# Kernel tuning notes

Hardware: AMD Instinct MI355X
Metric: run time of the kernel (lower is better)

## Reference

```python
import jax, jax.numpy as jnp
from jax import lax
import numpy as np

B, Q, T, C = 64, 900, 100, 92
W_CLASS, W_BBOX, W_GIOU = 1.0, 1.0, 1.0


def to_corners(b):
    cx, cy, w, h = b[..., 0], b[..., 1], b[..., 2], b[..., 3]
    return jnp.stack([cx - 0.5 * w, cy - 0.5 * h, cx + 0.5 * w, cy + 0.5 * h], axis=-1)


def generalized_iou(b1, b2):
    # b1 [Q,4], b2 [T,4] in corner format -> pairwise GIoU [Q,T]
    a1 = (b1[:, 2] - b1[:, 0]) * (b1[:, 3] - b1[:, 1])
    a2 = (b2[:, 2] - b2[:, 0]) * (b2[:, 3] - b2[:, 1])
    lt = jnp.maximum(b1[:, None, :2], b2[None, :, :2])
    rb = jnp.minimum(b1[:, None, 2:], b2[None, :, 2:])
    wh = jnp.clip(rb - lt, 0.0)
    inter = wh[..., 0] * wh[..., 1]
    union = a1[:, None] + a2[None, :] - inter
    iou = inter / union
    lt_e = jnp.minimum(b1[:, None, :2], b2[None, :, :2])
    rb_e = jnp.maximum(b1[:, None, 2:], b2[None, :, 2:])
    wh_e = jnp.clip(rb_e - lt_e, 0.0)
    area_e = wh_e[..., 0] * wh_e[..., 1]
    return iou - (area_e - union) / area_e


def cost_matrix(logits, pred_bbox, tgt_labels, tgt_bbox):
    conf = jax.nn.softmax(logits, axis=-1)                                  # [B,Q,C]
    cost_class = -jax.vmap(lambda c, l: c[:, l])(conf, tgt_labels)          # [B,Q,T]
    cost_bbox = jnp.sum(jnp.abs(pred_bbox[:, :, None, :] - tgt_bbox[:, None, :, :]), axis=-1)
    cost_giou = -jax.vmap(generalized_iou)(to_corners(pred_bbox), to_corners(tgt_bbox))
    return W_BBOX * cost_bbox + W_CLASS * cost_class + W_GIOU * cost_giou   # [B,Q,T]


def solve_lsa(cost):
    # Jonker-Volgenant shortest-augmenting-path optimal assignment.
    # cost [n, m] with n <= m; assigns every row to a distinct column.
    n, m = cost.shape
    INF = jnp.asarray(1e9, cost.dtype)

    def assign_row(i, carry):
        u, v, p = carry        # u [n+1], v [m+1] potentials; p [m+1]: row assigned to col (0=free)
        p = p.at[0].set(i + 1)
        minv0 = jnp.full(m + 1, INF, cost.dtype)
        used0 = jnp.zeros(m + 1, bool)
        way0 = jnp.zeros(m + 1, jnp.int32)

        def cond(s):
            j0, u, v, p, minv, used, way = s
            return p[j0] != 0

        def body(s):
            j0, u, v, p, minv, used, way = s
            used = used.at[j0].set(True)
            i0 = p[j0]
            cur = cost[i0 - 1] - u[i0] - v[1:]          # reduced costs over cols 1..m
            cur = jnp.where(used[1:], INF, cur)
            better = cur < minv[1:]
            minv = minv.at[1:].set(jnp.where(better, cur, minv[1:]))
            way = way.at[1:].set(jnp.where(better, j0, way[1:]))
            masked = jnp.where(used[1:], INF, minv[1:])
            j1 = jnp.argmin(masked).astype(jnp.int32) + 1
            delta = masked[j1 - 1]
            u = u.at[p].add(jnp.where(used, delta, jnp.zeros((), cost.dtype)))
            v = v - jnp.where(used, delta, jnp.zeros((), cost.dtype))
            minv = minv - jnp.where(used, jnp.zeros((), cost.dtype), delta)
            return j1, u, v, p, minv, used, way

        j0, u, v, p, _, _, way = lax.while_loop(
            cond, body, (jnp.int32(0), u, v, p, minv0, used0, way0))

        def aug_cond(s):
            jj, p = s
            return jj != 0

        def aug_body(s):
            jj, p = s
            j1 = way[jj]
            p = p.at[jj].set(p[j1])
            return j1, p

        _, p = lax.while_loop(aug_cond, aug_body, (j0, p))
        return u, v, p

    u0 = jnp.zeros(n + 1, cost.dtype)
    v0 = jnp.zeros(m + 1, cost.dtype)
    p0 = jnp.zeros(m + 1, jnp.int32)
    _, _, p = lax.fori_loop(0, n, assign_row, (u0, v0, p0))
    # column (0-based) assigned to each row i
    q = jnp.argmax(p[1:, None] == (jnp.arange(n, dtype=jnp.int32) + 1)[None, :], axis=0)
    order = jnp.argsort(q)
    return q[order].astype(jnp.int32), order.astype(jnp.int32)


def setup_inputs() -> dict:
    key = jax.random.key(0)
    k1, k2, k3, k4 = jax.random.split(key, 4)
    return {
        'logits': jax.random.normal(k1, (B, Q, C), jnp.float32),
        'pred_bbox': jax.random.uniform(k2, (B, Q, 4), jnp.float32),
        'tgt_labels': jax.random.randint(k3, (B, T), 0, C, jnp.int32),
        'tgt_bbox': jax.random.uniform(k4, (B, T, 4), jnp.float32),
    }


def reference(logits, pred_bbox, tgt_labels, tgt_bbox):
    cost = cost_matrix(logits, pred_bbox, tgt_labels, tgt_bbox)   # [B,Q,T]
    # scipy solves the [Q,T] problem (Q > T): transpose so rows (targets) <= cols (queries).
    row_ind, col_ind = jax.vmap(lambda c: solve_lsa(c.T))(cost)
    # row_ind: query indices (ascending), col_ind: matched target indices, per image.
    return cost, row_ind, col_ind
```

## Files before the change

kernel.cpp:

```cpp
#include <hip/hip_runtime.h>
#include <cmath>

#define Bq 64
#define Qn 900
#define Tn 100
#define Cn 92
#define INFN 1e9f
#define QT 64
#define NQT 15

__device__ inline unsigned fkey(float x) {
    unsigned u = __float_as_uint(x);
    return (u & 0x80000000u) ? ~u : (u | 0x80000000u);
}
__device__ inline float unfkey(unsigned k) {
    unsigned u = (k & 0x80000000u) ? (k & 0x7FFFFFFFu) : ~k;
    return __uint_as_float(u);
}

__device__ inline unsigned wave_min_u32(unsigned x) {
    unsigned t;
#define DPPSTEP(ctrl)                                                          \
    t = (unsigned)__builtin_amdgcn_update_dpp((int)0xFFFFFFFF, (int)x, ctrl,   \
                                              0xF, 0xF, false);                \
    x = (t < x) ? t : x;
    DPPSTEP(0x111)
    DPPSTEP(0x112)
    DPPSTEP(0x114)
    DPPSTEP(0x118)
    DPPSTEP(0x142)
    DPPSTEP(0x143)
#undef DPPSTEP
    return (unsigned)__builtin_amdgcn_readlane((int)x, 63);
}

__global__ __launch_bounds__(256) void cost_fused_kernel(
        const float* __restrict__ logits,
        const float* __restrict__ pred_bbox,
        const int*   __restrict__ tgt_labels,
        const float* __restrict__ tgt_bbox,
        float* __restrict__ cost,
        float* __restrict__ costT,
        unsigned long long* __restrict__ tilemin)
{
    const int b   = blockIdx.y;
    const int q0  = blockIdx.x * QT;
    const int nq  = (q0 + QT <= Qn) ? QT : (Qn - q0);
    const int tid = threadIdx.x;

    __shared__ float prob[QT * Cn];
    __shared__ float pb_s[QT][4];
    __shared__ float tb_s[Tn][4];
    __shared__ int   lab_s[Tn];
    __shared__ float ctile[QT][Tn + 1];

    const float* lg_src = logits + ((size_t)b * Qn + q0) * Cn;
    for (int idx = tid; idx < nq * Cn; idx += 256) prob[idx] = lg_src[idx];
    for (int idx = tid; idx < nq * 4; idx += 256)
        ((float*)pb_s)[idx] = pred_bbox[((size_t)b * Qn + q0) * 4 + idx];
    for (int idx = tid; idx < Tn * 4; idx += 256)
        ((float*)tb_s)[idx] = tgt_bbox[(size_t)b * Tn * 4 + idx];
    for (int idx = tid; idx < Tn; idx += 256)
        lab_s[idx] = tgt_labels[b * Tn + idx];
    __syncthreads();

    const int g = tid >> 2, l4 = tid & 3;
    if (g < nq) {
        float mx = -3.0e38f;
        for (int c = l4; c < Cn; c += 4) mx = fmaxf(mx, prob[g * Cn + c]);
        mx = fmaxf(mx, __shfl_xor(mx, 1));
        mx = fmaxf(mx, __shfl_xor(mx, 2));
        float s = 0.0f;
        for (int c = l4; c < Cn; c += 4) {
            float e = expf(prob[g * Cn + c] - mx);
            prob[g * Cn + c] = e;
            s += e;
        }
        s += __shfl_xor(s, 1);
        s += __shfl_xor(s, 2);
        float inv = 1.0f / s;
        for (int c = l4; c < Cn; c += 4) prob[g * Cn + c] *= inv;
    }
    __syncthreads();

    const int total = nq * Tn;
    float* cdst = cost + (size_t)b * Qn * Tn + (size_t)q0 * Tn;
    for (int flat = tid; flat < total; flat += 256) {
        int q = flat / Tn, tt = flat - q * Tn;
        float pcx = pb_s[q][0], pcy = pb_s[q][1], pw = pb_s[q][2], ph = pb_s[q][3];
        float tcx = tb_s[tt][0], tcy = tb_s[tt][1], tw = tb_s[tt][2], th = tb_s[tt][3];

        float cclass = -prob[q * Cn + lab_s[tt]];
        float cbbox  = fabsf(pcx - tcx) + fabsf(pcy - tcy)
                     + fabsf(pw - tw)  + fabsf(ph - th);

        float px1 = pcx - 0.5f * pw, py1 = pcy - 0.5f * ph;
        float px2 = pcx + 0.5f * pw, py2 = pcy + 0.5f * ph;
        float tx1 = tcx - 0.5f * tw, ty1 = tcy - 0.5f * th;
        float tx2 = tcx + 0.5f * tw, ty2 = tcy + 0.5f * th;

        float a1 = (px2 - px1) * (py2 - py1);
        float a2 = (tx2 - tx1) * (ty2 - ty1);
        float iw = fmaxf(fminf(px2, tx2) - fmaxf(px1, tx1), 0.0f);
        float ih = fmaxf(fminf(py2, ty2) - fmaxf(py1, ty1), 0.0f);
        float inter = iw * ih;
        float uni = a1 + a2 - inter;
        float iou = inter / uni;
        float ew = fmaxf(fmaxf(px2, tx2) - fminf(px1, tx1), 0.0f);
        float eh = fmaxf(fmaxf(py2, ty2) - fminf(py1, ty1), 0.0f);
        float ae = ew * eh;
        float val = cbbox + cclass - (iou - (ae - uni) / ae);

        cdst[flat] = val;
        ctile[q][tt] = val;
    }
    __syncthreads();

    if (costT) {
        float* tdst = costT + (size_t)b * Qn * Tn + q0;
        if (nq == QT) {
            for (int flat = tid; flat < QT * Tn; flat += 256) {
                int r = flat >> 6, c = flat & 63;
                tdst[(size_t)r * Qn + c] = ctile[c][r];
            }
        } else {
            for (int flat = tid; flat < nq * Tn; flat += 256) {
                int r = flat / nq, c = flat - r * nq;
                tdst[(size_t)r * Qn + c] = ctile[c][r];
            }
        }
    }
    if (tilemin && tid < Tn) {
        float bvv = 3.0e38f; int bq = 0;
        for (int q = 0; q < nq; ++q) {
            float x = ctile[q][tid];
            if (x < bvv) { bvv = x; bq = q; }
        }
        tilemin[((size_t)b * NQT + blockIdx.x) * Tn + tid] =
            ((unsigned long long)fkey(bvv) << 32) | (unsigned)(q0 + bq);
    }
}

template<bool TM>
__global__ __launch_bounds__(256) void jv_kernel(
        const float* __restrict__ costT,
        const unsigned long long* __restrict__ tilemin,
        float* __restrict__ out)
{
    const int b    = blockIdx.x;
    const int tid  = threadIdx.x;
    const int lane = tid & 63;
    const int wv   = tid >> 6;

    __shared__ int   p_lds[Qn + 1];
    __shared__ int   way_lds[1024];
    __shared__ float u_lds[Tn + 1];
    __shared__ int   amin_lds[Tn];
    __shared__ unsigned char asg[Tn];
    __shared__ int   freelist[Tn];
    __shared__ int   nfree_s;
    __shared__ int   qarr[Tn];

    for (int j = tid; j <= Qn; j += 256) p_lds[j] = 0;
    if (tid == 0) nfree_s = 0;
    __syncthreads();

    const float* cb = costT + (size_t)b * Qn * Tn;

    if (TM) {
        if (tid < Tn) {
            unsigned long long best = ~0ull;
            for (int t = 0; t < NQT; ++t) {
                unsigned long long v = tilemin[((size_t)b * NQT + t) * Tn + tid];
                if (v < best) best = v;
            }
            u_lds[tid + 1] = unfkey((unsigned)(best >> 32));
            amin_lds[tid]  = (int)(best & 0xFFFFFFFFu);
        }
    } else {
        for (int r = wv; r < Tn; r += 4) {
            float bv = 3.0e38f; int bj = 0x3fffffff;
            #pragma unroll
            for (int k = 0; k < 15; ++k) {
                int c = lane + 64 * k;
                if (c < Qn) {
                    float x = cb[(size_t)r * Qn + c];
                    if (x < bv) { bv = x; bj = c; }
                }
            }
            #pragma unroll
            for (int off = 1; off < 64; off <<= 1) {
                float ov = __shfl_xor(bv, off);
                int   oj = __shfl_xor(bj, off);
                if (ov < bv || (ov == bv && oj < bj)) { bv = ov; bj = oj; }
            }
            if (lane == 0) { u_lds[r + 1] = bv; amin_lds[r] = bj; }
        }
    }
    __syncthreads();

    if (tid < Tn) {
        int j = amin_lds[tid];
        int old = atomicCAS(&p_lds[j + 1], 0, tid + 1);
        asg[tid] = (old == 0) ? 1 : 0;
    }
    __syncthreads();
    if (tid < Tn && !asg[tid]) {
        int s = atomicAdd(&nfree_s, 1);
        freelist[s] = tid;
    }
    __syncthreads();
    const int nfree = nfree_s;

    if (wv == 0 && nfree > 0) {
        const int cbase = lane << 4;
        float v_r[16], minv_r[16], rc[16], rn[16];
        #pragma unroll
        for (int k = 0; k < 16; ++k) v_r[k] = 0.0f;

#define LOADROW(dst, row1)                                                     \
        {                                                                      \
            const float* rp = cb + (size_t)((row1) - 1) * Qn;                  \
            if (cbase + 16 <= Qn) {                                            \
                _Pragma("unroll")                                              \
                for (int w4 = 0; w4 < 4; ++w4) {                               \
                    float4 f = *(const float4*)(rp + cbase + 4 * w4);          \
                    dst[4*w4+0] = f.x; dst[4*w4+1] = f.y;                      \
                    dst[4*w4+2] = f.z; dst[4*w4+3] = f.w;                      \
                }                                                              \
            } else {                                                           \
                _Pragma("unroll")                                              \
                for (int k = 0; k < 16; ++k)                                   \
                    dst[k] = (cbase + k < Qn) ? rp[cbase + k] : 3.0e38f;       \
            }                                                                  \
        }

        for (int s = 0; s < nfree; ++s) {
            const int ri = freelist[s];
            unsigned um = 0;
            #pragma unroll
            for (int k = 0; k < 16; ++k) minv_r[k] = 3.0e38f;
            int i0 = ri + 1, j0 = 0;
            if (lane == 0) p_lds[0] = i0;
            LOADROW(rc, i0);
            float ui0 = u_lds[i0];

            for (int it = 0; it < Tn + 2; ++it) {
                if (j0 > 0) {
                    int cc = j0 - 1;
                    if ((cc >> 4) == lane) um |= 1u << (cc & 15);
                }
                float bv = 3.0e38f; int bj = 0;
                #pragma unroll
                for (int k = 0; k < 16; ++k) {
                    int c = cbase + k;
                    if (c < Qn && !((um >> k) & 1u)) {
                        float cur = rc[k] - ui0 - v_r[k];
                        if (cur < minv_r[k]) {
                            minv_r[k] = cur;
                            way_lds[(k << 6) | lane] = j0;
                        }
                        if (minv_r[k] < bv) { bv = minv_r[k]; bj = c; }
                    }
                }
                unsigned tk = fkey(bv);
                unsigned gk = wave_min_u32(tk);
                unsigned long long msk = __ballot(tk == gk);
                int src = __ffsll(msk) - 1;
                int bestj = __shfl(bj, src) + 1;
                float delta = __shfl(bv, src);
                int bp = p_lds[bestj];

                float un = 0.0f;
                if (bp != 0) { LOADROW(rn, bp); un = u_lds[bp]; }

                if (lane == 0) u_lds[ri + 1] += delta;
                #pragma unroll
                for (int k = 0; k < 16; ++k) {
                    int c = cbase + k;
                    if (c < Qn) {
                        if ((um >> k) & 1u) {
                            v_r[k] -= delta;
                            u_lds[p_lds[c + 1]] += delta;
                        } else {
                            minv_r[k] -= delta;
                        }
                    }
                }
                j0 = bestj;
                if (bp == 0) break;
                i0 = bp; ui0 = un;
                #pragma unroll
                for (int k = 0; k < 16; ++k) rc[k] = rn[k];
            }

            if (lane == 0) {
                int jj = j0;
                while (jj != 0) {
                    int cc = jj - 1;
                    int j1 = way_lds[((cc & 15) << 6) | (cc >> 4)];
                    p_lds[jj] = p_lds[j1];
                    jj = j1;
                }
            }
            __threadfence_block();
        }
#undef LOADROW
    }
    __syncthreads();

    for (int j = tid + 1; j <= Qn; j += 256) {
        int r = p_lds[j];
        if (r) qarr[r - 1] = j - 1;
    }
    __syncthreads();

    float* out_row = out + (size_t)Bq * Qn * Tn + (size_t)b * Tn;
    float* out_col = out_row + (size_t)Bq * Tn;
    for (int i = tid; i < Tn; i += 256) {
        int qi = qarr[i];
        int rank = 0;
        for (int jj = 0; jj < Tn; ++jj) rank += (qarr[jj] < qi) ? 1 : 0;
        out_row[rank] = (float)qi;
        out_col[rank] = (float)i;
    }
}

__global__ __launch_bounds__(256) void jv_compat_kernel(
        const float* __restrict__ cost,
        float* __restrict__ out)
{
    const int b    = blockIdx.x;
    const int tid  = threadIdx.x;
    const int lane = tid & 63;
    const int wv   = tid >> 6;
    const bool act = (tid < Qn / 4);

    __shared__ int   p_lds[Qn + 1];
    __shared__ int   way_lds[Qn + 1];
    __shared__ float u_lds[Tn + 1];
    __shared__ int   amin_lds[Tn];
    __shared__ unsigned char asg[Tn];
    __shared__ int   freelist[Tn];
    __shared__ int   nfree_s;
    __shared__ float redv[2][4];
    __shared__ int   redj[2][4];
    __shared__ int   qarr[Tn];

    for (int j = tid; j <= Qn; j += 256) p_lds[j] = 0;
    if (tid == 0) nfree_s = 0;
    __syncthreads();

    const float* cb = cost + (size_t)b * Qn * Tn;

    for (int r = wv; r < Tn; r += 4) {
        float bv = 3.0e38f; int bj = 0x3fffffff;
        #pragma unroll
        for (int k = 0; k < 15; ++k) {
            int c = lane + 64 * k;
            if (c < Qn) {
                float x = cb[(size_t)c * Tn + r];
                if (x < bv) { bv = x; bj = c; }
            }
        }
        #pragma unroll
        for (int off = 1; off < 64; off <<= 1) {
            float ov = __shfl_xor(bv, off);
            int   oj = __shfl_xor(bj, off);
            if (ov < bv || (ov == bv && oj < bj)) { bv = ov; bj = oj; }
        }
        if (lane == 0) { u_lds[r + 1] = bv; amin_lds[r] = bj; }
    }
    __syncthreads();

    if (tid < Tn) {
        int j = amin_lds[tid];
        int old = atomicCAS(&p_lds[j + 1], 0, tid + 1);
        asg[tid] = (old == 0) ? 1 : 0;
    }
    __syncthreads();
    if (tid < Tn && !asg[tid]) {
        int s = atomicAdd(&nfree_s, 1);
        freelist[s] = tid;
    }
    __syncthreads();
    const int nfree = nfree_s;

    const int cbase = 4 * tid;
    float varr[4] = {0.0f, 0.0f, 0.0f, 0.0f};

    for (int s = 0; s < nfree; ++s) {
        const int ri = freelist[s];
        float minv[4] = {INFN, INFN, INFN, INFN};
        unsigned um = 0;
        int i0 = ri + 1, j0 = 0;
        if (tid == 0) p_lds[0] = i0;

        float c0v = 0, c1v = 0, c2v = 0, c3v = 0;
        if (act) {
            const float* cp = cb + (i0 - 1);
            c0v = cp[(size_t)cbase * Tn];       c1v = cp[(size_t)(cbase + 1) * Tn];
            c2v = cp[(size_t)(cbase + 2) * Tn]; c3v = cp[(size_t)(cbase + 3) * Tn];
        }
        float ui0 = u_lds[i0];

        for (int it = 0; it < Tn + 2; ++it) {
            if (j0 > 0 && act) {
                int cc = j0 - 1;
                if ((cc >> 2) == tid) um |= 1u << (cc & 3);
            }
            float bv = 3.0e9f; int bj = 0x3fffffff;
            if (act) {
                float crr[4] = {c0v, c1v, c2v, c3v};
                #pragma unroll
                for (int k = 0; k < 4; ++k) {
                    if (!((um >> k) & 1u)) {
                        float cur = crr[k] - ui0 - varr[k];
                        if (cur < minv[k]) { minv[k] = cur; way_lds[cbase + k + 1] = j0; }
                        if (minv[k] < bv) { bv = minv[k]; bj = cbase + k + 1; }
                    }
                }
            }
            #pragma unroll
            for (int off = 1; off < 64; off <<= 1) {
                float ov = __shfl_xor(bv, off);
                int   oj = __shfl_xor(bj, off);
                if (ov < bv || (ov == bv && oj < bj)) { bv = ov; bj = oj; }
            }
            const int par = it & 1;
            if (lane == 0) { redv[par][wv] = bv; redj[par][wv] = bj; }
            __syncthreads();
            float delta = redv[par][0]; int bestj = redj[par][0];
            #pragma unroll
            for (int w = 1; w < 4; ++w) {
                float ov = redv[par][w]; int oj = redj[par][w];
                if (ov < delta || (ov == delta && oj < bestj)) { delta = ov; bestj = oj; }
            }
            const int bp = p_lds[bestj];

            float ui_n = 0.0f, n0 = 0, n1 = 0, n2 = 0, n3 = 0;
            if (bp != 0) {
                if (act) {
                    const float* cp = cb + (bp - 1);
                    n0 = cp[(size_t)cbase * Tn];       n1 = cp[(size_t)(cbase + 1) * Tn];
                    n2 = cp[(size_t)(cbase + 2) * Tn]; n3 = cp[(size_t)(cbase + 3) * Tn];
                }
                ui_n = u_lds[bp];
            }

            if (tid == 0) u_lds[ri + 1] += delta;
            if (act) {
                #pragma unroll
                for (int k = 0; k < 4; ++k) {
                    if ((um >> k) & 1u) {
                        varr[k] -= delta;
                        u_lds[p_lds[cbase + k + 1]] += delta;
                    } else {
                        minv[k] -= delta;
                    }
                }
            }
            j0 = bestj;
            if (bp == 0) break;
            i0 = bp; ui0 = ui_n;
            c0v = n0; c1v = n1; c2v = n2; c3v = n3;
        }

        if (tid == 0) {
            int jj = j0;
            while (jj != 0) { int j1 = way_lds[jj]; p_lds[jj] = p_lds[j1]; jj = j1; }
        }
        __syncthreads();
    }

    for (int j = tid + 1; j <= Qn; j += 256) {
        int r = p_lds[j];
        if (r) qarr[r - 1] = j - 1;
    }
    __syncthreads();

    float* out_row = out + (size_t)Bq * Qn * Tn + (size_t)b * Tn;
    float* out_col = out_row + (size_t)Bq * Tn;
    for (int i = tid; i < Tn; i += 256) {
        int qi = qarr[i];
        int rank = 0;
        for (int jj = 0; jj < Tn; ++jj) rank += (qarr[jj] < qi) ? 1 : 0;
        out_row[rank] = (float)qi;
        out_col[rank] = (float)i;
    }
}

extern "C" void kernel_launch(void* const* d_in, const int* in_sizes, int n_in,
                              void* d_out, int out_size, void* d_ws, size_t ws_size,
                              hipStream_t stream) {
    const float* logits     = (const float*)d_in[0];
    const float* pred_bbox  = (const float*)d_in[1];
    const int*   tgt_labels = (const int*)d_in[2];
    const float* tgt_bbox   = (const float*)d_in[3];
    float* out = (float*)d_out;

    const size_t needT  = (size_t)Bq * Qn * Tn * sizeof(float);
    const size_t needTM = needT + (size_t)Bq * NQT * Tn * 8 + 4096;

    if (ws_size >= needTM) {
        float* costT = (float*)d_ws;
        unsigned long long* tilemin = (unsigned long long*)((char*)d_ws + needT);
        hipLaunchKernelGGL(cost_fused_kernel, dim3(NQT, Bq), dim3(256), 0, stream,
                           logits, pred_bbox, tgt_labels, tgt_bbox, out, costT, tilemin);
        hipLaunchKernelGGL((jv_kernel<true>), dim3(Bq), dim3(256), 0, stream,
                           costT, tilemin, out);
    } else if (ws_size >= needT) {
        float* costT = (float*)d_ws;
        hipLaunchKernelGGL(cost_fused_kernel, dim3(NQT, Bq), dim3(256), 0, stream,
                           logits, pred_bbox, tgt_labels, tgt_bbox, out, costT,
                           (unsigned long long*)nullptr);
        hipLaunchKernelGGL((jv_kernel<false>), dim3(Bq), dim3(256), 0, stream,
                           costT, (const unsigned long long*)nullptr, out);
    } else {
        hipLaunchKernelGGL(cost_fused_kernel, dim3(NQT, Bq), dim3(256), 0, stream,
                           logits, pred_bbox, tgt_labels, tgt_bbox, out,
                           (float*)nullptr, (unsigned long long*)nullptr);
        hipLaunchKernelGGL(jv_compat_kernel, dim3(Bq), dim3(256), 0, stream,
                           out, out);
    }
}
```

Baseline: 111.0 us.

## Add auction-style augmenting row reduction before shortest-path augmentation

Adds a Jonker-Volgenant augmenting row reduction phase that processes free rows using the best and second-best reduced costs. It updates column potentials and bumps rows off their columns, bounded by a step cap. The phase is meant to cut the number of rows needing the expensive shortest-augmenting-path search. The cost is extra wave-wide shuffle reductions per step, and the ordering of assignments can change, so ties could be resolved differently.

```diff
diff --git a/kernel.cpp b/kernel.cpp
--- a/kernel.cpp
+++ b/kernel.cpp
@@ -8,6 +8,7 @@
 #define INFN 1e9f
 #define QT 64
 #define NQT 15
+#define MAXARR 300
 
 __device__ inline unsigned fkey(float x) {
     unsigned u = __float_as_uint(x);
@@ -235,7 +236,53 @@
             }                                                                  \
         }
 
-        for (int s = 0; s < nfree; ++s) {
+        int sp = nfree;
+        for (int steps = 0; sp > 0 && steps < MAXARR; ++steps) {
+            const int i = freelist[sp - 1];
+            sp--;
+            LOADROW(rc, i + 1);
+
+            float m1 = 3.0e38f, m2 = 3.0e38f;
+            int j1i = 0x3fffffff, j2i = 0x3fffffff;
+            #pragma unroll
+            for (int k = 0; k < 16; ++k) {
+                int c = cbase + k;
+                if (c < Qn) {
+                    float cur = rc[k] - v_r[k];
+                    if (cur < m1) { m2 = m1; j2i = j1i; m1 = cur; j1i = c; }
+                    else if (cur < m2) { m2 = cur; j2i = c; }
+                }
+            }
+            #pragma unroll
+            for (int off = 1; off < 64; off <<= 1) {
+                float om1 = __shfl_xor(m1, off), om2 = __shfl_xor(m2, off);
+                int   oj1 = __shfl_xor(j1i, off), oj2 = __shfl_xor(j2i, off);
+                if (om1 < m1 || (om1 == m1 && oj1 < j1i)) {
+                    float lm = m1; int lj = j1i;
+                    m1 = om1; j1i = oj1;
+                    if (om2 < lm || (om2 == lm && oj2 < lj)) { m2 = om2; j2i = oj2; }
+                    else { m2 = lm; j2i = lj; }
+                } else {
+                    if (om1 < m2 || (om1 == m2 && oj1 < j2i)) { m2 = om1; j2i = oj1; }
+                }
+            }
+
+            if (lane == 0) u_lds[i + 1] = m2;
+            int jj = j1i;
+            if (m1 < m2) {
+                if ((j1i >> 4) == lane) v_r[j1i & 15] -= (m2 - m1);
+            } else {
+                if (p_lds[j1i + 1] != 0) jj = j2i;
+            }
+            const int kown = p_lds[jj + 1];
+            if (lane == 0) p_lds[jj + 1] = i + 1;
+            if (kown != 0) {
+                if (lane == 0) freelist[sp] = kown - 1;
+                sp++;
+            }
+        }
+
+        for (int s = 0; s < sp; ++s) {
             const int ri = freelist[s];
             unsigned um = 0;
             #pragma unroll
```

Result: slower. 148.6 us (+33.8%).

## Use Dijkstra-style lazy potential updates in JV augmenting search

Applied to the files above, without the earlier changes.

Rewrites the per-row augmenting search to track absolute distances instead of reduced minv, deferring the dual potential updates on u and v until the sink is found instead of applying them every iteration. Column owners are cached in registers (p_r) so the next row comes from a shuffle rather than an LDS lookup, and the separate next-row prefetch buffer is dropped. This removes the per-iteration update loop and the scattered u_lds atomics-like writes, in exchange for a new indexing convention for p and way that must stay consistent.

```diff
diff --git a/kernel.cpp b/kernel.cpp
--- a/kernel.cpp
+++ b/kernel.cpp
@@ -152,7 +152,7 @@
     const int lane = tid & 63;
     const int wv   = tid >> 6;
 
-    __shared__ int   p_lds[Qn + 1];
+    __shared__ int   p0_lds[1024];
     __shared__ int   way_lds[1024];
     __shared__ float u_lds[Tn + 1];
     __shared__ int   amin_lds[Tn];
@@ -161,7 +161,7 @@
     __shared__ int   nfree_s;
     __shared__ int   qarr[Tn];
 
-    for (int j = tid; j <= Qn; j += 256) p_lds[j] = 0;
+    for (int j = tid; j < 1024; j += 256) p0_lds[j] = 0;
     if (tid == 0) nfree_s = 0;
     __syncthreads();
 
@@ -201,7 +201,7 @@
 
     if (tid < Tn) {
         int j = amin_lds[tid];
-        int old = atomicCAS(&p_lds[j + 1], 0, tid + 1);
+        int old = atomicCAS(&p0_lds[j], 0, tid + 1);
         asg[tid] = (old == 0) ? 1 : 0;
     }
     __syncthreads();
@@ -214,7 +214,8 @@
 
     if (wv == 0 && nfree > 0) {
         const int cbase = lane << 4;
-        float v_r[16], minv_r[16], rc[16], rn[16];
+        float v_r[16], dist_r[16], rc[16];
+        int   p_r[16];
         #pragma unroll
         for (int k = 0; k < 16; ++k) v_r[k] = 0.0f;
 
@@ -237,81 +238,85 @@
 
         for (int s = 0; s < nfree; ++s) {
             const int ri = freelist[s];
+
+            {
+                const int4* pp = (const int4*)(p0_lds + cbase);
+                int4 a = pp[0], bb = pp[1], cc4 = pp[2], dd4 = pp[3];
+                p_r[0]=a.x;  p_r[1]=a.y;  p_r[2]=a.z;  p_r[3]=a.w;
+                p_r[4]=bb.x; p_r[5]=bb.y; p_r[6]=bb.z; p_r[7]=bb.w;
+                p_r[8]=cc4.x; p_r[9]=cc4.y; p_r[10]=cc4.z; p_r[11]=cc4.w;
+                p_r[12]=dd4.x; p_r[13]=dd4.y; p_r[14]=dd4.z; p_r[15]=dd4.w;
+            }
+            #pragma unroll
+            for (int k = 0; k < 16; ++k) dist_r[k] = 3.0e38f;
             unsigned um = 0;
-            #pragma unroll
-            for (int k = 0; k < 16; ++k) minv_r[k] = 3.0e38f;
-            int i0 = ri + 1, j0 = 0;
-            if (lane == 0) p_lds[0] = i0;
+            int   i0   = ri + 1;
+            float d0   = 0.0f;
+            int   jenc = 0;
+            int   sink0 = -1;
+            float dstar = 0.0f;
+
             LOADROW(rc, i0);
             float ui0 = u_lds[i0];
 
             for (int it = 0; it < Tn + 2; ++it) {
-                if (j0 > 0) {
-                    int cc = j0 - 1;
-                    if ((cc >> 4) == lane) um |= 1u << (cc & 15);
-                }
-                float bv = 3.0e38f; int bj = 0;
+                const float sft = d0 - ui0;
+                float bv = 3.0e38f; int bj = 0x7fffffff; int bown = 0;
                 #pragma unroll
                 for (int k = 0; k < 16; ++k) {
                     int c = cbase + k;
                     if (c < Qn && !((um >> k) & 1u)) {
-                        float cur = rc[k] - ui0 - v_r[k];
-                        if (cur < minv_r[k]) {
-                            minv_r[k] = cur;
-                            way_lds[(k << 6) | lane] = j0;
+                        float cand = sft + rc[k] - v_r[k];
+                        if (cand < dist_r[k]) {
+                            dist_r[k] = cand;
+                            way_lds[(k << 6) | lane] = jenc;
                         }
-                        if (minv_r[k] < bv) { bv = minv_r[k]; bj = c; }
+                        if (dist_r[k] < bv) { bv = dist_r[k]; bj = c; bown = p_r[k]; }
                     }
                 }
                 unsigned tk = fkey(bv);
                 unsigned gk = wave_min_u32(tk);
                 unsigned long long msk = __ballot(tk == gk);
                 int src = __ffsll(msk) - 1;
-                int bestj = __shfl(bj, src) + 1;
+                int   bestj = __shfl(bj, src);
                 float delta = __shfl(bv, src);
-                int bp = p_lds[bestj];
-
-                float un = 0.0f;
-                if (bp != 0) { LOADROW(rn, bp); un = u_lds[bp]; }
-
-                if (lane == 0) u_lds[ri + 1] += delta;
-                #pragma unroll
-                for (int k = 0; k < 16; ++k) {
-                    int c = cbase + k;
-                    if (c < Qn) {
-                        if ((um >> k) & 1u) {
-                            v_r[k] -= delta;
-                            u_lds[p_lds[c + 1]] += delta;
-                        } else {
-                            minv_r[k] -= delta;
-                        }
-                    }
-                }
-                j0 = bestj;
-                if (bp == 0) break;
-                i0 = bp; ui0 = un;
-                #pragma unroll
-                for (int k = 0; k < 16; ++k) rc[k] = rn[k];
-            }
-
-            if (lane == 0) {
-                int jj = j0;
-                while (jj != 0) {
-                    int cc = jj - 1;
-                    int j1 = way_lds[((cc & 15) << 6) | (cc >> 4)];
-                    p_lds[jj] = p_lds[j1];
-                    jj = j1;
-                }
-            }
-            __threadfence_block();
+                int   bp    = __shfl(bown, src);
+
+                if (bp == 0) { sink0 = bestj; dstar = delta; break; }
+
+                if ((bestj >> 4) == lane) um |= 1u << (bestj & 15);
+                LOADROW(rc, bp);
+                ui0 = u_lds[bp];
+                d0 = delta; i0 = bp; jenc = bestj + 1;
+            }
+
+            if (lane == 0) u_lds[ri + 1] += dstar;
+            #pragma unroll
+            for (int k = 0; k < 16; ++k) {
+                if ((um >> k) & 1u) {
+                    float dd = dstar - dist_r[k];
+                    v_r[k] -= dd;
+                    u_lds[p_r[k]] += dd;
+                }
+            }
+
+            if (lane == 0 && sink0 >= 0) {
+                int jj = sink0;
+                while (true) {
+                    int w = way_lds[((jj & 15) << 6) | (jj >> 4)];
+                    if (w == 0) { p0_lds[jj] = ri + 1; break; }
+                    p0_lds[jj] = p0_lds[w - 1];
+                    jj = w - 1;
+                }
+            }
         }
 #undef LOADROW
     }
     __syncthreads();
 
-    for (int j = tid + 1; j <= Qn; j += 256) {
-        int r = p_lds[j];
-        if (r) qarr[r - 1] = j - 1;
+    for (int c = tid; c < Qn; c += 256) {
+        int r = p0_lds[c];
+        if (r) qarr[r - 1] = c;
     }
     __syncthreads();
 
```

New measurement: 103.8 us. -6.5%, faster.
